# Kernel optimization log

Measured on AMD Instinct MI355X. Metric: run time of the kernel, lower is better.

The kernel has to match this reference:

```python
import jax, jax.numpy as jnp
import numpy as np

H = 16          # hidden_size
L = 24          # num_layers
LEN_TRAIN = 96
LEN_PRED = 48
B = 256         # leading dim of input (acts as TIME axis for the LSTMs, see notes)


def setup_inputs() -> dict:
    key = jax.random.key(0)
    ks = jax.random.split(key, 16)
    s = 1.0 / np.sqrt(H)  # PyTorch LSTM/Linear init scale
    u = lambda k, shp: jax.random.uniform(k, shp, jnp.float32, -s, s)
    return {
        "x": jax.random.normal(ks[0], (B, 1, LEN_TRAIN), jnp.float32),
        # lstm1: layer0 input_size=1, layers 1..23 input_size=2H
        "W_ih0_1": u(ks[1], (2, 4 * H, 1)),
        "W_ih_1": u(ks[2], (L - 1, 2, 4 * H, 2 * H)),
        "W_hh_1": u(ks[3], (L, 2, 4 * H, H)),
        "b_ih_1": u(ks[4], (L, 2, 4 * H)),
        "b_hh_1": u(ks[5], (L, 2, 4 * H)),
        # lstm2: all layers input_size=2H
        "W_ih_2": u(ks[6], (L, 2, 4 * H, 2 * H)),
        "W_hh_2": u(ks[7], (L, 2, 4 * H, H)),
        "b_ih_2": u(ks[8], (L, 2, 4 * H)),
        "b_hh_2": u(ks[9], (L, 2, 4 * H)),
        "fc1_w": u(ks[10], (1000, 2 * LEN_PRED * H)),
        "fc1_b": u(ks[11], (1000,)),
        "fc2_w": u(ks[12], (LEN_PRED, 1000)),
        "fc2_b": u(ks[13], (LEN_PRED,)),
    }


def _lstm_dir(x, Wih, Whh, bih, bhh, reverse):
    # x: (T, N, in). Precompute input-gate GEMM over whole sequence.
    xg = jnp.einsum("tni,gi->tng", x, Wih) + bih + bhh  # (T, N, 4H)

    def step(carry, g_in):
        h, c = carry
        g = g_in + h @ Whh.T
        i, f, gg, o = jnp.split(g, 4, axis=-1)  # PyTorch gate order i,f,g,o
        c = jax.nn.sigmoid(f) * c + jax.nn.sigmoid(i) * jnp.tanh(gg)
        h = jax.nn.sigmoid(o) * jnp.tanh(c)
        return (h, c), h

    N = x.shape[1]
    init = (jnp.zeros((N, H), x.dtype), jnp.zeros((N, H), x.dtype))
    _, hs = jax.lax.scan(step, init, xg, reverse=reverse)
    return hs  # (T, N, H), in original time order


def _bilstm_stack(x, Wih_per_layer, Whh, bih, bhh):
    for l in range(Whh.shape[0]):
        Wih = Wih_per_layer[l]
        fwd = _lstm_dir(x, Wih[0], Whh[l, 0], bih[l, 0], bhh[l, 0], False)
        bwd = _lstm_dir(x, Wih[1], Whh[l, 1], bih[l, 1], bhh[l, 1], True)
        x = jnp.concatenate([fwd, bwd], axis=-1)  # (T, N, 2H)
    return x


def reference(x, W_ih0_1, W_ih_1, W_hh_1, b_ih_1, b_hh_1,
              W_ih_2, W_hh_2, b_ih_2, b_hh_2,
              fc1_w, fc1_b, fc2_w, fc2_b):
    xp = jnp.transpose(x, (0, 2, 1))  # (B, 96, 1); dim0 is the LSTM time axis (batch_first=False quirk)
    wih1 = [W_ih0_1] + [W_ih_1[i] for i in range(L - 1)]
    h = _bilstm_stack(xp, wih1, W_hh_1, b_ih_1, b_hh_1)      # (B, 96, 2H)
    x1 = h[:, -LEN_PRED:, :]                                  # (B, 48, 2H)
    wih2 = [W_ih_2[i] for i in range(L)]
    h2 = _bilstm_stack(x1, wih2, W_hh_2, b_ih_2, b_hh_2)      # (B, 48, 2H)
    z = h2 + x1
    flat = z.reshape(z.shape[0], -1)                          # (B, 1536)
    y = jax.nn.relu(flat @ fc1_w.T + fc1_b) @ fc2_w.T + fc2_b # (B, 48)
    return jnp.transpose(y.reshape(y.shape[0], LEN_PRED, 1), (0, 2, 1))  # (B, 1, 48)
```

## Files before the change

### kernel.cpp

```cpp
#include <hip/hip_runtime.h>


template <int SEL>
__device__ __forceinline__ float quad_bcast(float v) {
  return __int_as_float(__builtin_amdgcn_update_dpp(
      0, __float_as_int(v), SEL * 0x55, 0xF, 0xF, true));
}

template <int IN_SZ, int N>
__global__ __launch_bounds__(256) void lstm_layer(
    const float* __restrict__ xin, float* __restrict__ xout,
    const float* __restrict__ Wih, const float* __restrict__ Whh,
    const float* __restrict__ bih, const float* __restrict__ bhh,
    int t_stride, int n_off) {
  __shared__ float xg[256 * 64];

  const int tid = threadIdx.x;
  const int lane = tid & 63;
  const int w = tid >> 6;
  const int d = blockIdx.x / N;
  const int n = blockIdx.x % N;

  {
    const int r = lane;
    const float bias = bih[d * 64 + r] + bhh[d * 64 + r];
    if constexpr (IN_SZ == 1) {
      const float xv =
          xin[(size_t)(w * 64 + lane) * t_stride + (n + n_off)];
      const float wih0 = Wih[d * 64 + r];
      const int xvb = __float_as_int(xv);
      for (int ti = 0; ti < 64; ++ti) {
        const float xs = __int_as_float(__builtin_amdgcn_readlane(xvb, ti));
        xg[(w * 64 + ti) * 64 + r] = fmaf(wih0, xs, bias);
      }
    } else {
      const int r8 = lane >> 3;
      const int c = lane & 7;
      const float* gbase = xin + (size_t)(n + n_off) * 32 + c * 4;
      float4 v[8];
#pragma unroll
      for (int i = 0; i < 8; ++i) {
        const int t = w * 64 + i * 8 + r8;
        v[i] = *reinterpret_cast<const float4*>(gbase + (size_t)t * t_stride);
      }
#pragma unroll
      for (int i = 0; i < 8; ++i) {
        const int t = w * 64 + i * 8 + r8;
        *reinterpret_cast<float4*>(&xg[t * 64 + 32 + c * 4]) = v[i];
      }
      float wih[32];
      const float4* wp =
          reinterpret_cast<const float4*>(Wih + (size_t)(d * 64 + r) * 32);
#pragma unroll
      for (int q = 0; q < 8; ++q) {
        const float4 t4 = wp[q];
        wih[4 * q + 0] = t4.x;
        wih[4 * q + 1] = t4.y;
        wih[4 * q + 2] = t4.z;
        wih[4 * q + 3] = t4.w;
      }
      for (int ti = 0; ti < 64; ++ti) {
        const int t = w * 64 + ti;
        const float4* xr = reinterpret_cast<const float4*>(&xg[t * 64 + 32]);
        float a0 = bias, a1 = 0.f, a2 = 0.f, a3 = 0.f;
#pragma unroll
        for (int q = 0; q < 8; ++q) {
          const float4 xv = xr[q];
          a0 = fmaf(wih[4 * q + 0], xv.x, a0);
          a1 = fmaf(wih[4 * q + 1], xv.y, a1);
          a2 = fmaf(wih[4 * q + 2], xv.z, a2);
          a3 = fmaf(wih[4 * q + 3], xv.w, a3);
        }
        xg[t * 64 + r] = (a0 + a1) + (a2 + a3);
      }
    }
  }
  __syncthreads();

  if (w == 0) {
    const int j = lane >> 2;
    const int g = lane & 3;
    const int r = g * 16 + j;

    float whh[16];
#pragma unroll
    for (int k = 0; k < 16; ++k) whh[k] = Whh[(d * 64 + r) * 16 + k];

    const float s_ = (g == 2) ? 2.885390082f : -1.442695041f;
    const float m_ = (g == 2) ? -2.0f : 1.0f;
    const float b_ = (g == 2) ? 1.0f : 0.0f;

    float hs[16];
#pragma unroll
    for (int k = 0; k < 16; ++k) hs[k] = 0.f;
    float c = 0.f;

    const int dt = d ? -1 : 1;
    int t = d ? 255 : 0;
    float cur0 = xg[t * 64 + r];
    float cur1 = xg[(t + dt) * 64 + r];

#define LSTM_STEP(CUR, TT)                                              \
  {                                                                     \
    float a0 = (CUR), a1 = 0.f, a2 = 0.f, a3 = 0.f;                     \
    _Pragma("unroll") for (int k = 0; k < 16; k += 4) {                 \
      a0 = fmaf(whh[k + 0], hs[k + 0], a0);                             \
      a1 = fmaf(whh[k + 1], hs[k + 1], a1);                             \
      a2 = fmaf(whh[k + 2], hs[k + 2], a2);                             \
      a3 = fmaf(whh[k + 3], hs[k + 3], a3);                             \
    }                                                                   \
    const float gv = (a0 + a1) + (a2 + a3);                             \
    const float e = __builtin_amdgcn_exp2f(s_ * gv);                    \
    const float v = fmaf(m_, __builtin_amdgcn_rcpf(1.0f + e), b_);      \
    const float si = quad_bcast<0>(v);                                  \
    const float sf = quad_bcast<1>(v);                                  \
    const float tg = quad_bcast<2>(v);                                  \
    const float so = quad_bcast<3>(v);                                  \
    c = fmaf(sf, c, si * tg);                                           \
    const float e2 = __builtin_amdgcn_exp2f(2.885390082f * c);          \
    const float th = fmaf(-2.0f, __builtin_amdgcn_rcpf(1.0f + e2), 1.0f); \
    const float h = so * th;                                            \
    xg[(TT)*64 + lane] = h;    \
    const int hb = __float_as_int(h);                                   \
    _Pragma("unroll") for (int k = 0; k < 16; ++k) hs[k] =              \
        __int_as_float(__builtin_amdgcn_readlane(hb, 4 * k));           \
  }

    for (int tt = 0; tt < 256; tt += 2) {
      const float nx0 = xg[((t + 2 * dt) & 255) * 64 + r];
      LSTM_STEP(cur0, t)
      const float nx1 = xg[((t + 3 * dt) & 255) * 64 + r];
      LSTM_STEP(cur1, t + dt)
      cur0 = nx0;
      cur1 = nx1;
      t += 2 * dt;
    }
#undef LSTM_STEP
  }
  __syncthreads();

  {
    const int q4 = tid & 3;
    const int tb = tid >> 2;
#pragma unroll
    for (int p = 0; p < 4; ++p) {
      const int t = p * 64 + tb;
      float4 v;
      v.x = xg[t * 64 + 16 * q4 + 0];
      v.y = xg[t * 64 + 16 * q4 + 4];
      v.z = xg[t * 64 + 16 * q4 + 8];
      v.w = xg[t * 64 + 16 * q4 + 12];
      *reinterpret_cast<float4*>(xout + ((size_t)t * N + n) * 32 + d * 16 +
                                 q4 * 4) = v;
    }
  }
}

__global__ __launch_bounds__(256) void fc1_kernel(
    const float* __restrict__ h2,
    const float* __restrict__ x1b,
    const float* __restrict__ w1, const float* __restrict__ b1,
    float* __restrict__ y1) {
  __shared__ float Zs[16][68];
  __shared__ float Ws[16][68];
  const int tid = threadIdx.x;
  const int m0 = blockIdx.x * 64;
  const int b0 = blockIdx.y * 64;
  const int rr = tid >> 2;
  const int c4 = (tid & 3) * 4;
  const int tx = tid & 15, ty = tid >> 4;

  float acc[4][4];
#pragma unroll
  for (int i = 0; i < 4; ++i)
#pragma unroll
    for (int jj = 0; jj < 4; ++jj) acc[i][jj] = 0.f;

  const bool wvalid = (m0 + rr) < 1000;
  const float* zr = h2 + (size_t)(b0 + rr) * 1536 + c4;
  const float* zr2 = x1b + (size_t)(b0 + rr) * 3072 + 1536 + c4;
  const float* wr = w1 + (size_t)(m0 + rr) * 1536 + c4;

  float4 za = *reinterpret_cast<const float4*>(zr);
  float4 zb = *reinterpret_cast<const float4*>(zr2);
  float4 wv = wvalid ? *reinterpret_cast<const float4*>(wr)
                     : make_float4(0.f, 0.f, 0.f, 0.f);

  for (int k0 = 0; k0 < 1536; k0 += 16) {
    Zs[c4 + 0][rr] = za.x + zb.x;
    Zs[c4 + 1][rr] = za.y + zb.y;
    Zs[c4 + 2][rr] = za.z + zb.z;
    Zs[c4 + 3][rr] = za.w + zb.w;
    Ws[c4 + 0][rr] = wv.x;
    Ws[c4 + 1][rr] = wv.y;
    Ws[c4 + 2][rr] = wv.z;
    Ws[c4 + 3][rr] = wv.w;
    if (k0 + 16 < 1536) {
      za = *reinterpret_cast<const float4*>(zr + k0 + 16);
      zb = *reinterpret_cast<const float4*>(zr2 + k0 + 16);
      if (wvalid) wv = *reinterpret_cast<const float4*>(wr + k0 + 16);
    }
    __syncthreads();
#pragma unroll
    for (int kk = 0; kk < 16; ++kk) {
      const float4 av = *reinterpret_cast<const float4*>(&Zs[kk][ty * 4]);
      const float4 bv = *reinterpret_cast<const float4*>(&Ws[kk][tx * 4]);
      const float a_[4] = {av.x, av.y, av.z, av.w};
      const float b_[4] = {bv.x, bv.y, bv.z, bv.w};
#pragma unroll
      for (int i = 0; i < 4; ++i)
#pragma unroll
        for (int jj = 0; jj < 4; ++jj)
          acc[i][jj] = fmaf(a_[i], b_[jj], acc[i][jj]);
    }
    __syncthreads();
  }
#pragma unroll
  for (int i = 0; i < 4; ++i) {
    const int b = b0 + ty * 4 + i;
#pragma unroll
    for (int jj = 0; jj < 4; ++jj) {
      const int m = m0 + tx * 4 + jj;
      if (m < 1000) {
        float vo = acc[i][jj] + b1[m];
        y1[(size_t)b * 1000 + m] = vo > 0.f ? vo : 0.f;
      }
    }
  }
}

__global__ __launch_bounds__(64) void fc2_kernel(
    const float* __restrict__ y1, const float* __restrict__ w2,
    const float* __restrict__ b2, float* __restrict__ out) {
  __shared__ float ys[1000];
  const int b = blockIdx.x;
  for (int k = threadIdx.x; k < 1000; k += 64) ys[k] = y1[(size_t)b * 1000 + k];
  __syncthreads();
  const int p = threadIdx.x;
  if (p < 48) {
    float a0 = b2[p], a1 = 0.f, a2 = 0.f, a3 = 0.f;
    const float* wr = w2 + (size_t)p * 1000;
    for (int k = 0; k < 1000; k += 4) {
      const float4 wv = *reinterpret_cast<const float4*>(wr + k);
      a0 = fmaf(ys[k + 0], wv.x, a0);
      a1 = fmaf(ys[k + 1], wv.y, a1);
      a2 = fmaf(ys[k + 2], wv.z, a2);
      a3 = fmaf(ys[k + 3], wv.w, a3);
    }
    out[(size_t)b * 48 + p] = (a0 + a1) + (a2 + a3);
  }
}

extern "C" void kernel_launch(void* const* d_in, const int* in_sizes, int n_in,
                              void* d_out, int out_size, void* d_ws,
                              size_t ws_size, hipStream_t stream) {
  const float* x = (const float*)d_in[0];
  const float* W_ih0_1 = (const float*)d_in[1];
  const float* W_ih_1 = (const float*)d_in[2];
  const float* W_hh_1 = (const float*)d_in[3];
  const float* b_ih_1 = (const float*)d_in[4];
  const float* b_hh_1 = (const float*)d_in[5];
  const float* W_ih_2 = (const float*)d_in[6];
  const float* W_hh_2 = (const float*)d_in[7];
  const float* b_ih_2 = (const float*)d_in[8];
  const float* b_hh_2 = (const float*)d_in[9];
  const float* fc1_w = (const float*)d_in[10];
  const float* fc1_b = (const float*)d_in[11];
  const float* fc2_w = (const float*)d_in[12];
  const float* fc2_b = (const float*)d_in[13];

  float* ws = (float*)d_ws;
  float* buf0 = ws;
  float* buf1 = ws + 786432;
  float* y1 = ws + 2 * 786432;
  float* q0 = buf0;
  float* q1 = buf0 + 393216;

  lstm_layer<1, 96><<<192, 256, 0, stream>>>(x, buf0, W_ih0_1, W_hh_1, b_ih_1,
                                             b_hh_1, 96, 0);
  for (int l = 1; l < 24; ++l) {
    const float* in = (l & 1) ? buf0 : buf1;
    float* outb = (l & 1) ? buf1 : buf0;
    lstm_layer<32, 96><<<192, 256, 0, stream>>>(
        in, outb, W_ih_1 + (size_t)(l - 1) * 4096, W_hh_1 + (size_t)l * 2048,
        b_ih_1 + l * 128, b_hh_1 + l * 128, 3072, 0);
  }
  lstm_layer<32, 48><<<96, 256, 0, stream>>>(buf1, q0, W_ih_2, W_hh_2, b_ih_2,
                                             b_hh_2, 3072, 48);
  for (int l = 1; l < 24; ++l) {
    const float* in = (l & 1) ? q0 : q1;
    float* outb = (l & 1) ? q1 : q0;
    lstm_layer<32, 48><<<96, 256, 0, stream>>>(
        in, outb, W_ih_2 + (size_t)l * 4096, W_hh_2 + (size_t)l * 2048,
        b_ih_2 + l * 128, b_hh_2 + l * 128, 1536, 0);
  }
  fc1_kernel<<<dim3(16, 4), 256, 0, stream>>>(q1, buf1, fc1_w, fc1_b, y1);
  fc2_kernel<<<256, 64, 0, stream>>>(y1, fc2_w, fc2_b, (float*)d_out);
}
```

Baseline: 2.241 ms.

## Fuse all 48 LSTM layers into one persistent kernel with pairwise flag sync

Replaces 48 per-layer launches with a single persistent kernel of 192 blocks. Each sequence index n is handled by a forward and a backward block, and the two exchange their halves of each layer's output through global memory, synchronising with acquire/release flags. Blocks for n<48 stop after stack 1, while blocks for n>=48 carry on through stack 2. Only the partner half is reloaded per layer, since the own half stays in LDS. This removes launch overhead and full-grid serialisation between layers, at the cost of spin-waiting, a layout change in fc1's input loads, and dropping fc1's register prefetch.

Result: slower. 2.892 ms (+29.0%).

```diff
diff --git a/kernel.cpp b/kernel.cpp
--- a/kernel.cpp
+++ b/kernel.cpp
@@ -7,50 +7,68 @@
       0, __float_as_int(v), SEL * 0x55, 0xF, 0xF, true));
 }
 
-template <int IN_SZ, int N>
-__global__ __launch_bounds__(256) void lstm_layer(
-    const float* __restrict__ xin, float* __restrict__ xout,
-    const float* __restrict__ Wih, const float* __restrict__ Whh,
-    const float* __restrict__ bih, const float* __restrict__ bhh,
-    int t_stride, int n_off) {
+__global__ __launch_bounds__(256) void lstm_fused(
+    const float* __restrict__ x, const float* __restrict__ W_ih0_1,
+    const float* __restrict__ W_ih_1, const float* __restrict__ W_hh_1,
+    const float* __restrict__ b_ih_1, const float* __restrict__ b_hh_1,
+    const float* __restrict__ W_ih_2, const float* __restrict__ W_hh_2,
+    const float* __restrict__ b_ih_2, const float* __restrict__ b_hh_2,
+    float* __restrict__ hb, float* __restrict__ x1b, float* __restrict__ h2b,
+    int* __restrict__ flags) {
   __shared__ float xg[256 * 64];
 
   const int tid = threadIdx.x;
   const int lane = tid & 63;
   const int w = tid >> 6;
-  const int d = blockIdx.x / N;
-  const int n = blockIdx.x % N;
-
-  {
-    const int r = lane;
-    const float bias = bih[d * 64 + r] + bhh[d * 64 + r];
-    if constexpr (IN_SZ == 1) {
-      const float xv =
-          xin[(size_t)(w * 64 + lane) * t_stride + (n + n_off)];
-      const float wih0 = Wih[d * 64 + r];
-      const int xvb = __float_as_int(xv);
-      for (int ti = 0; ti < 64; ++ti) {
-        const float xs = __int_as_float(__builtin_amdgcn_readlane(xvb, ti));
-        xg[(w * 64 + ti) * 64 + r] = fmaf(wih0, xs, bias);
-      }
+  const int bid = blockIdx.x;
+  const int n = bid >> 1;
+  const int d = bid & 1;
+  const int pid = bid ^ 1;
+  const int d16 = d * 16;
+  const int jj = lane >> 2, g = lane & 3;
+
+  const int nlay = (n < 48) ? 24 : 48;
+
+  for (int L = 0; L < nlay; ++L) {
+    const bool s2 = (L >= 24);
+    const int l = s2 ? (L - 24) : L;
+
+    if (L > 0) {
+      if (tid == 0) {
+        while (__hip_atomic_load(&flags[pid], __ATOMIC_ACQUIRE,
+                                 __HIP_MEMORY_SCOPE_AGENT) < L)
+          __builtin_amdgcn_s_sleep(2);
+      }
+      __syncthreads();
+      const float* src =
+          (L == 24)
+              ? (x1b + (((size_t)(1 - d) * 48 + (n - 48)) * 256) * 16)
+              : (hb + ((((size_t)((L - 1) & 1) * 2 + (1 - d)) * 96 + n) * 256) *
+                          16);
+      const int c = (tid & 3) * 4;
+#pragma unroll
+      for (int p = 0; p < 4; ++p) {
+        const int tt = (tid >> 2) + p * 64;
+        const float4 v =
+            *reinterpret_cast<const float4*>(src + (size_t)tt * 16 + c);
+        *reinterpret_cast<float4*>(&xg[tt * 64 + 32 + (1 - d) * 16 + c]) = v;
+      }
+      __syncthreads();
+    }
+
+    const int rL = lane;
+    const float* bih = s2 ? b_ih_2 : b_ih_1;
+    const float* bhh = s2 ? b_hh_2 : b_hh_1;
+    const float bias = bih[l * 128 + d * 64 + rL] + bhh[l * 128 + d * 64 + rL];
+    float wih[32];
+    float wih0 = 0.f;
+    if (L == 0) {
+      wih0 = W_ih0_1[d * 64 + rL];
     } else {
-      const int r8 = lane >> 3;
-      const int c = lane & 7;
-      const float* gbase = xin + (size_t)(n + n_off) * 32 + c * 4;
-      float4 v[8];
-#pragma unroll
-      for (int i = 0; i < 8; ++i) {
-        const int t = w * 64 + i * 8 + r8;
-        v[i] = *reinterpret_cast<const float4*>(gbase + (size_t)t * t_stride);
-      }
-#pragma unroll
-      for (int i = 0; i < 8; ++i) {
-        const int t = w * 64 + i * 8 + r8;
-        *reinterpret_cast<float4*>(&xg[t * 64 + 32 + c * 4]) = v[i];
-      }
-      float wih[32];
+      const float* Wih = s2 ? (W_ih_2 + (size_t)l * 4096)
+                            : (W_ih_1 + (size_t)(l - 1) * 4096);
       const float4* wp =
-          reinterpret_cast<const float4*>(Wih + (size_t)(d * 64 + r) * 32);
+          reinterpret_cast<const float4*>(Wih + ((size_t)d * 64 + rL) * 32);
 #pragma unroll
       for (int q = 0; q < 8; ++q) {
         const float4 t4 = wp[q];
@@ -59,106 +77,121 @@
         wih[4 * q + 2] = t4.z;
         wih[4 * q + 3] = t4.w;
       }
+    }
+
+    if (L == 0) {
+      const float xv = x[(size_t)tid * 96 + n];
+      xg[tid * 64 + 32] = xv;
+      __syncthreads();
+      for (int ti = 0; ti < 64; ++ti) {
+        const int t = w * 64 + ti;
+        const float xs = xg[t * 64 + 32];
+        xg[t * 64 + rL] = fmaf(wih0, xs, bias);
+      }
+    } else {
       for (int ti = 0; ti < 64; ++ti) {
         const int t = w * 64 + ti;
         const float4* xr = reinterpret_cast<const float4*>(&xg[t * 64 + 32]);
         float a0 = bias, a1 = 0.f, a2 = 0.f, a3 = 0.f;
 #pragma unroll
         for (int q = 0; q < 8; ++q) {
-          const float4 xv = xr[q];
-          a0 = fmaf(wih[4 * q + 0], xv.x, a0);
-          a1 = fmaf(wih[4 * q + 1], xv.y, a1);
-          a2 = fmaf(wih[4 * q + 2], xv.z, a2);
-          a3 = fmaf(wih[4 * q + 3], xv.w, a3);
+          const float4 xv4 = xr[q];
+          a0 = fmaf(wih[4 * q + 0], xv4.x, a0);
+          a1 = fmaf(wih[4 * q + 1], xv4.y, a1);
+          a2 = fmaf(wih[4 * q + 2], xv4.z, a2);
+          a3 = fmaf(wih[4 * q + 3], xv4.w, a3);
         }
-        xg[t * 64 + r] = (a0 + a1) + (a2 + a3);
-      }
-    }
-  }
-  __syncthreads();
-
-  if (w == 0) {
-    const int j = lane >> 2;
-    const int g = lane & 3;
-    const int r = g * 16 + j;
-
-    float whh[16];
-#pragma unroll
-    for (int k = 0; k < 16; ++k) whh[k] = Whh[(d * 64 + r) * 16 + k];
-
-    const float s_ = (g == 2) ? 2.885390082f : -1.442695041f;
-    const float m_ = (g == 2) ? -2.0f : 1.0f;
-    const float b_ = (g == 2) ? 1.0f : 0.0f;
-
-    float hs[16];
-#pragma unroll
-    for (int k = 0; k < 16; ++k) hs[k] = 0.f;
-    float c = 0.f;
-
-    const int dt = d ? -1 : 1;
-    int t = d ? 255 : 0;
-    float cur0 = xg[t * 64 + r];
-    float cur1 = xg[(t + dt) * 64 + r];
-
-#define LSTM_STEP(CUR, TT)                                              \
-  {                                                                     \
-    float a0 = (CUR), a1 = 0.f, a2 = 0.f, a3 = 0.f;                     \
-    _Pragma("unroll") for (int k = 0; k < 16; k += 4) {                 \
-      a0 = fmaf(whh[k + 0], hs[k + 0], a0);                             \
-      a1 = fmaf(whh[k + 1], hs[k + 1], a1);                             \
-      a2 = fmaf(whh[k + 2], hs[k + 2], a2);                             \
-      a3 = fmaf(whh[k + 3], hs[k + 3], a3);                             \
-    }                                                                   \
-    const float gv = (a0 + a1) + (a2 + a3);                             \
-    const float e = __builtin_amdgcn_exp2f(s_ * gv);                    \
-    const float v = fmaf(m_, __builtin_amdgcn_rcpf(1.0f + e), b_);      \
-    const float si = quad_bcast<0>(v);                                  \
-    const float sf = quad_bcast<1>(v);                                  \
-    const float tg = quad_bcast<2>(v);                                  \
-    const float so = quad_bcast<3>(v);                                  \
-    c = fmaf(sf, c, si * tg);                                           \
-    const float e2 = __builtin_amdgcn_exp2f(2.885390082f * c);          \
+        xg[t * 64 + rL] = (a0 + a1) + (a2 + a3);
+      }
+    }
+    __syncthreads();
+
+    if (w == 0) {
+      const int r = g * 16 + jj;
+      const float* Whh =
+          s2 ? (W_hh_2 + (size_t)l * 2048) : (W_hh_1 + (size_t)l * 2048);
+      float whh[16];
+#pragma unroll
+      for (int k = 0; k < 16; ++k) whh[k] = Whh[((size_t)d * 64 + r) * 16 + k];
+      const float s_ = (g == 2) ? 2.885390082f : -1.442695041f;
+      const float m_ = (g == 2) ? -2.0f : 1.0f;
+      const float b_ = (g == 2) ? 1.0f : 0.0f;
+      float hs[16];
+#pragma unroll
+      for (int k = 0; k < 16; ++k) hs[k] = 0.f;
+      float c = 0.f;
+      const int dt = d ? -1 : 1;
+      int t = d ? 255 : 0;
+      float cur0 = xg[t * 64 + r];
+      float cur1 = xg[(t + dt) * 64 + r];
+
+#define LSTM_STEP(CUR, TT)                                                \
+  {                                                                       \
+    float a0 = (CUR), a1 = 0.f, a2 = 0.f, a3 = 0.f;                       \
+    _Pragma("unroll") for (int k = 0; k < 16; k += 4) {                   \
+      a0 = fmaf(whh[k + 0], hs[k + 0], a0);                               \
+      a1 = fmaf(whh[k + 1], hs[k + 1], a1);                               \
+      a2 = fmaf(whh[k + 2], hs[k + 2], a2);                               \
+      a3 = fmaf(whh[k + 3], hs[k + 3], a3);                               \
+    }                                                                     \
+    const float gv = (a0 + a1) + (a2 + a3);                               \
+    const float e = __builtin_amdgcn_exp2f(s_ * gv);                      \
+    const float v = fmaf(m_, __builtin_amdgcn_rcpf(1.0f + e), b_);        \
+    const float si = quad_bcast<0>(v);                                    \
+    const float sf = quad_bcast<1>(v);                                    \
+    const float tg = quad_bcast<2>(v);                                    \
+    const float so = quad_bcast<3>(v);                                    \
+    c = fmaf(sf, c, si * tg);                                             \
+    const float e2 = __builtin_amdgcn_exp2f(2.885390082f * c);            \
     const float th = fmaf(-2.0f, __builtin_amdgcn_rcpf(1.0f + e2), 1.0f); \
-    const float h = so * th;                                            \
-    xg[(TT)*64 + lane] = h;    \
-    const int hb = __float_as_int(h);                                   \
-    _Pragma("unroll") for (int k = 0; k < 16; ++k) hs[k] =              \
-        __int_as_float(__builtin_amdgcn_readlane(hb, 4 * k));           \
-  }
-
-    for (int tt = 0; tt < 256; tt += 2) {
-      const float nx0 = xg[((t + 2 * dt) & 255) * 64 + r];
-      LSTM_STEP(cur0, t)
-      const float nx1 = xg[((t + 3 * dt) & 255) * 64 + r];
-      LSTM_STEP(cur1, t + dt)
-      cur0 = nx0;
-      cur1 = nx1;
-      t += 2 * dt;
-    }
+    const float h = so * th;                                              \
+    if (g == 0) xg[(TT)*64 + 32 + d16 + jj] = h;                          \
+    const int hbb = __float_as_int(h);                                    \
+    _Pragma("unroll") for (int k = 0; k < 16; ++k) hs[k] =                \
+        __int_as_float(__builtin_amdgcn_readlane(hbb, 4 * k));            \
+  }
+
+      for (int tt = 0; tt < 256; tt += 2) {
+        const float nx0 = xg[((t + 2 * dt) & 255) * 64 + r];
+        LSTM_STEP(cur0, t)
+        const float nx1 = xg[((t + 3 * dt) & 255) * 64 + r];
+        LSTM_STEP(cur1, t + dt)
+        cur0 = nx0;
+        cur1 = nx1;
+        t += 2 * dt;
+      }
 #undef LSTM_STEP
-  }
-  __syncthreads();
-
-  {
-    const int q4 = tid & 3;
-    const int tb = tid >> 2;
-#pragma unroll
-    for (int p = 0; p < 4; ++p) {
-      const int t = p * 64 + tb;
-      float4 v;
-      v.x = xg[t * 64 + 16 * q4 + 0];
-      v.y = xg[t * 64 + 16 * q4 + 4];
-      v.z = xg[t * 64 + 16 * q4 + 8];
-      v.w = xg[t * 64 + 16 * q4 + 12];
-      *reinterpret_cast<float4*>(xout + ((size_t)t * N + n) * 32 + d * 16 +
-                                 q4 * 4) = v;
+    }
+    __syncthreads();
+
+    float* dst;
+    if (L == 47)
+      dst = h2b + (((size_t)d * 48 + (n - 48)) * 256) * 16;
+    else if (L == 23 && n >= 48)
+      dst = x1b + (((size_t)d * 48 + (n - 48)) * 256) * 16;
+    else
+      dst = hb + ((((size_t)(L & 1) * 2 + d) * 96 + n) * 256) * 16;
+    {
+      const int c = (tid & 3) * 4;
+#pragma unroll
+      for (int p = 0; p < 4; ++p) {
+        const int tt = (tid >> 2) + p * 64;
+        const float4 v =
+            *reinterpret_cast<const float4*>(&xg[tt * 64 + 32 + d16 + c]);
+        *reinterpret_cast<float4*>(dst + (size_t)tt * 16 + c) = v;
+      }
+    }
+    __syncthreads();
+    if (tid == 0) {
+      __threadfence();
+      __hip_atomic_store(&flags[bid], L + 1, __ATOMIC_RELEASE,
+                         __HIP_MEMORY_SCOPE_AGENT);
     }
   }
 }
 
 __global__ __launch_bounds__(256) void fc1_kernel(
-    const float* __restrict__ h2,
-    const float* __restrict__ x1b,
+    const float* __restrict__ h2, const float* __restrict__ x1,
     const float* __restrict__ w1, const float* __restrict__ b1,
     float* __restrict__ y1) {
   __shared__ float Zs[16][68];
@@ -177,29 +210,24 @@
     for (int jj = 0; jj < 4; ++jj) acc[i][jj] = 0.f;
 
   const bool wvalid = (m0 + rr) < 1000;
-  const float* zr = h2 + (size_t)(b0 + rr) * 1536 + c4;
-  const float* zr2 = x1b + (size_t)(b0 + rr) * 3072 + 1536 + c4;
   const float* wr = w1 + (size_t)(m0 + rr) * 1536 + c4;
 
-  float4 za = *reinterpret_cast<const float4*>(zr);
-  float4 zb = *reinterpret_cast<const float4*>(zr2);
-  float4 wv = wvalid ? *reinterpret_cast<const float4*>(wr)
-                     : make_float4(0.f, 0.f, 0.f, 0.f);
-
   for (int k0 = 0; k0 < 1536; k0 += 16) {
+    const int k = k0 + c4;
+    const int n2 = k >> 5, dd = (k >> 4) & 1, j0 = k & 15;
+    const size_t off = (((size_t)dd * 48 + n2) * 256 + (b0 + rr)) * 16 + j0;
+    const float4 za = *reinterpret_cast<const float4*>(h2 + off);
+    const float4 zb = *reinterpret_cast<const float4*>(x1 + off);
     Zs[c4 + 0][rr] = za.x + zb.x;
     Zs[c4 + 1][rr] = za.y + zb.y;
     Zs[c4 + 2][rr] = za.z + zb.z;
     Zs[c4 + 3][rr] = za.w + zb.w;
+    float4 wv = make_float4(0.f, 0.f, 0.f, 0.f);
+    if (wvalid) wv = *reinterpret_cast<const float4*>(wr + k0);
     Ws[c4 + 0][rr] = wv.x;
     Ws[c4 + 1][rr] = wv.y;
     Ws[c4 + 2][rr] = wv.z;
     Ws[c4 + 3][rr] = wv.w;
-    if (k0 + 16 < 1536) {
-      za = *reinterpret_cast<const float4*>(zr + k0 + 16);
-      zb = *reinterpret_cast<const float4*>(zr2 + k0 + 16);
-      if (wvalid) wv = *reinterpret_cast<const float4*>(wr + k0 + 16);
-    }
     __syncthreads();
 #pragma unroll
     for (int kk = 0; kk < 16; ++kk) {
@@ -222,7 +250,7 @@
     for (int jj = 0; jj < 4; ++jj) {
       const int m = m0 + tx * 4 + jj;
       if (m < 1000) {
-        float vo = acc[i][jj] + b1[m];
+        const float vo = acc[i][jj] + b1[m];
         y1[(size_t)b * 1000 + m] = vo > 0.f ? vo : 0.f;
       }
     }
@@ -270,30 +298,16 @@
   const float* fc2_b = (const float*)d_in[13];
 
   float* ws = (float*)d_ws;
-  float* buf0 = ws;
-  float* buf1 = ws + 786432;
-  float* y1 = ws + 2 * 786432;
-  float* q0 = buf0;
-  float* q1 = buf0 + 393216;
-
-  lstm_layer<1, 96><<<192, 256, 0, stream>>>(x, buf0, W_ih0_1, W_hh_1, b_ih_1,
-                                             b_hh_1, 96, 0);
-  for (int l = 1; l < 24; ++l) {
-    const float* in = (l & 1) ? buf0 : buf1;
-    float* outb = (l & 1) ? buf1 : buf0;
-    lstm_layer<32, 96><<<192, 256, 0, stream>>>(
-        in, outb, W_ih_1 + (size_t)(l - 1) * 4096, W_hh_1 + (size_t)l * 2048,
-        b_ih_1 + l * 128, b_hh_1 + l * 128, 3072, 0);
-  }
-  lstm_layer<32, 48><<<96, 256, 0, stream>>>(buf1, q0, W_ih_2, W_hh_2, b_ih_2,
-                                             b_hh_2, 3072, 48);
-  for (int l = 1; l < 24; ++l) {
-    const float* in = (l & 1) ? q0 : q1;
-    float* outb = (l & 1) ? q1 : q0;
-    lstm_layer<32, 48><<<96, 256, 0, stream>>>(
-        in, outb, W_ih_2 + (size_t)l * 4096, W_hh_2 + (size_t)l * 2048,
-        b_ih_2 + l * 128, b_hh_2 + l * 128, 1536, 0);
-  }
-  fc1_kernel<<<dim3(16, 4), 256, 0, stream>>>(q1, buf1, fc1_w, fc1_b, y1);
+  int* flags = (int*)d_ws;
+  float* hbuf = ws + 256;
+  float* x1b = hbuf + 1572864;
+  float* h2b = x1b + 393216;
+  float* y1 = h2b + 393216;
+
+  hipMemsetAsync(flags, 0, 1024, stream);
+  lstm_fused<<<192, 256, 0, stream>>>(x, W_ih0_1, W_ih_1, W_hh_1, b_ih_1,
+                                      b_hh_1, W_ih_2, W_hh_2, b_ih_2, b_hh_2,
+                                      hbuf, x1b, h2b, flags);
+  fc1_kernel<<<dim3(16, 4), 256, 0, stream>>>(h2b, x1b, fc1_w, fc1_b, y1);
   fc2_kernel<<<256, 64, 0, stream>>>(y1, fc2_w, fc2_b, (float*)d_out);
 }
```
